# Performance work log

Hardware: AMD Instinct MI355X
Metric: run time of the kernel (lower is better)

The kernel has to match this reference:

```python
import jax, jax.numpy as jnp
import numpy as np

B, T, H = 32, 2000, 512      # batch, encoder frames, d_model
L = 256                      # max label length (padded output tokens)
THRESHOLD = 0.95


def setup_inputs() -> dict:
    key = jax.random.key(0)
    k1, k2, k3 = jax.random.split(key, 3)
    hidden = jax.random.normal(k1, (B, T, H), dtype=jnp.float32)
    alphas = jax.random.uniform(k2, (B, T), dtype=jnp.float32)
    target_lengths = jax.random.randint(k3, (B,), 64, L + 1)
    return {"hidden": hidden, "alphas": alphas, "target_lengths": target_lengths}


def _cif(hidden, alphas):
    # Continuous integrate-and-fire scan over time.
    Bt, Tt, Ht = hidden.shape

    def step(carry, xs):
        integrate, frame = carry          # [B], [B,H]
        alpha, h = xs                     # [B], [B,H]
        dist_completion = 1.0 - integrate
        integrate = integrate + alpha
        fire = integrate >= THRESHOLD     # [B] bool
        cur = jnp.where(fire, dist_completion, alpha)
        remainds = alpha - cur
        frame_out = frame + cur[:, None] * h
        integ_next = jnp.where(fire, integrate - 1.0, integrate)
        frame_next = jnp.where(fire[:, None], remainds[:, None] * h, frame_out)
        return (integ_next, frame_next), (frame_out, fire)

    init = (jnp.zeros((Bt,), hidden.dtype), jnp.zeros((Bt, Ht), hidden.dtype))
    _, (frames, fires) = jax.lax.scan(step, init, (alphas.T, jnp.swapaxes(hidden, 0, 1)))
    frames = jnp.swapaxes(frames, 0, 1)   # [B,T,H] accumulated frame at each step
    fires = fires.T                        # [B,T] fire events

    # Gather fired frames into padded [B, L, H] token tensor (vectorized scatter).
    tok = jnp.cumsum(fires.astype(jnp.int32), axis=1) - 1   # token index per fired frame
    valid = fires & (tok >= 0) & (tok < L)
    out = jnp.zeros((Bt, L, Ht), hidden.dtype)
    b_idx = jnp.arange(Bt)[:, None]
    out = out.at[b_idx, jnp.clip(tok, 0, L - 1)].add(
        frames * valid[..., None].astype(hidden.dtype))
    return out


def reference(hidden, alphas, target_lengths):
    # Rescale alphas so each row sums to target length (noise term omitted).
    num = target_lengths.astype(alphas.dtype)
    alphas = alphas * (num / alphas.sum(-1))[:, None]
    return _cif(hidden, alphas)
```

## Files before the change

kernel.cpp:

```cpp
#include <hip/hip_runtime.h>

#define BB 32
#define TT 2000
#define TTP 2048
#define HH 512
#define LL 256
#define THRESH 0.95f


__global__ __launch_bounds__(256) void cif_scan_kernel(
    const float* __restrict__ alphas, const int* __restrict__ tlen,
    float* __restrict__ w_self, float* __restrict__ w_next,
    int* __restrict__ fire_pos, int* __restrict__ nfires)
{
    const int b = blockIdx.x;
    __shared__ float sa[TTP];
    __shared__ double red[256];

    const float* arow = alphas + b * TT;
    double s = 0.0;
    for (int t = threadIdx.x; t < TT; t += 256) {
        float a = arow[t];
        sa[t] = a;
        s += (double)a;
    }
    if (threadIdx.x < TTP - TT) sa[TT + threadIdx.x] = 0.0f;
    red[threadIdx.x] = s;
    __syncthreads();
    for (int off = 128; off > 0; off >>= 1) {
        if (threadIdx.x < off) red[threadIdx.x] += red[threadIdx.x + off];
        __syncthreads();
    }
    const float sumf = (float)red[0];
    const float scale = (float)tlen[b] / sumf;
    for (int t = threadIdx.x; t < TT; t += 256) sa[t] = sa[t] * scale;
    __syncthreads();

    if (threadIdx.x == 0) {
        const float4* sa4 = (const float4*)sa;
        float4* ws4 = (float4*)(w_self + b * TT);
        float4* wn4 = (float4*)(w_next + b * TT);
        int* fp = fire_pos + b * LL;
        float integ = 0.0f;
        int nf = 0;

        float4 buf[16];
        #pragma unroll
        for (int i = 0; i < 16; ++i) buf[i] = sa4[i];

        for (int c = 0; c < 32; ++c) {
            float4 nbuf[16];
            if (c < 31) {
                #pragma unroll
                for (int i = 0; i < 16; ++i) nbuf[i] = sa4[(c + 1) * 16 + i];
            }
            #pragma unroll
            for (int i = 0; i < 16; ++i) {
                const int g = c * 16 + i;
                if (g < TT / 4) {
                    const float av[4] = {buf[i].x, buf[i].y, buf[i].z, buf[i].w};
                    float wsv[4], wnv[4];
                    #pragma unroll
                    for (int j = 0; j < 4; ++j) {
                        const float a = av[j];
                        const float dist = 1.0f - integ;
                        float ii = integ + a;
                        const bool fire = (ii >= THRESH);
                        wsv[j] = fire ? dist : a;
                        wnv[j] = fire ? (a - wsv[j]) : 0.0f;
                        if (fire) {
                            if (nf < LL) fp[nf] = g * 4 + j;
                            nf++;
                            ii -= 1.0f;
                        }
                        integ = ii;
                    }
                    ws4[g] = make_float4(wsv[0], wsv[1], wsv[2], wsv[3]);
                    wn4[g] = make_float4(wnv[0], wnv[1], wnv[2], wnv[3]);
                }
            }
            #pragma unroll
            for (int i = 0; i < 16; ++i) buf[i] = nbuf[i];
        }
        nfires[b] = (nf < LL) ? nf : LL;
    }
}

__global__ __launch_bounds__(128) void cif_gather_kernel(
    const float* __restrict__ hidden,
    const float* __restrict__ w_self, const float* __restrict__ w_next,
    const int* __restrict__ fire_pos, const int* __restrict__ nfires,
    float* __restrict__ out)
{
    const int l = blockIdx.x;
    const int b = blockIdx.y;
    const int tid = threadIdx.x;

    float4 acc = make_float4(0.f, 0.f, 0.f, 0.f);
    const int F = nfires[b];
    if (l < F) {
        const int e = fire_pos[b * LL + l];
        const float* hb = hidden + (size_t)b * TT * HH + (size_t)tid * 4;
        const float* wsb = w_self + b * TT;
        int t0;
        if (l == 0) {
            t0 = 0;
        } else {
            const int sprev = fire_pos[b * LL + l - 1];
            const float w = w_next[b * TT + sprev];
            const float4 hv0 = *(const float4*)(hb + (size_t)sprev * HH);
            acc.x = w * hv0.x; acc.y = w * hv0.y; acc.z = w * hv0.z; acc.w = w * hv0.w;
            t0 = sprev + 1;
        }
        int t = t0;
        float w = wsb[t];
        float4 hv = *(const float4*)(hb + (size_t)t * HH);
        while (t < e) {
            const float wN = wsb[t + 1];
            const float4 hN = *(const float4*)(hb + (size_t)(t + 1) * HH);
            acc.x += w * hv.x; acc.y += w * hv.y;
            acc.z += w * hv.z; acc.w += w * hv.w;
            w = wN; hv = hN; ++t;
        }
        acc.x += w * hv.x; acc.y += w * hv.y;
        acc.z += w * hv.z; acc.w += w * hv.w;
    }
    *(float4*)(out + ((size_t)b * LL + l) * HH + (size_t)tid * 4) = acc;
}

extern "C" void kernel_launch(void* const* d_in, const int* in_sizes, int n_in,
                              void* d_out, int out_size, void* d_ws, size_t ws_size,
                              hipStream_t stream) {
    const float* hidden = (const float*)d_in[0];
    const float* alphas = (const float*)d_in[1];
    const int*   tlen   = (const int*)d_in[2];
    float* out = (float*)d_out;

    float* w_self = (float*)d_ws;
    float* w_next = w_self + BB * TT;
    int* fire_pos = (int*)(w_next + BB * TT);
    int* nfires   = fire_pos + BB * LL;

    cif_scan_kernel<<<BB, 256, 0, stream>>>(alphas, tlen, w_self, w_next,
                                            fire_pos, nfires);
    cif_gather_kernel<<<dim3(LL, BB), 128, 0, stream>>>(hidden, w_self, w_next,
                                                        fire_pos, nfires, out);
}
```

Measured before the change: 300.3 us.

## Run CIF scan as one lane per batch row and record compact fire events

The scan kernel becomes a single block that first reduces the alpha sums for all rows, then gives each of 32 lanes one batch row to scan sequentially from global memory with a prefetch buffer. Instead of writing per-frame self and next weights, it stores one compact record per fire holding the position, the completion weight and the remainder. The gather kernel recomputes the interior weights from the alphas and the scale. This cuts workspace writes and moves the serial scans into one wave running side by side, but all rows now share a single CU, and alpha loads come from global memory rather than LDS.

```diff
diff --git a/kernel.cpp b/kernel.cpp
--- a/kernel.cpp
+++ b/kernel.cpp
@@ -2,7 +2,6 @@
 
 #define BB 32
 #define TT 2000
-#define TTP 2048
 #define HH 512
 #define LL 256
 #define THRESH 0.95f
@@ -10,87 +9,90 @@
 
 __global__ __launch_bounds__(256) void cif_scan_kernel(
     const float* __restrict__ alphas, const int* __restrict__ tlen,
-    float* __restrict__ w_self, float* __restrict__ w_next,
-    int* __restrict__ fire_pos, int* __restrict__ nfires)
+    float* __restrict__ scale_out, int* __restrict__ nfires,
+    int4* __restrict__ rec)
 {
-    const int b = blockIdx.x;
-    __shared__ float sa[TTP];
-    __shared__ double red[256];
+    __shared__ double red[8][256];
+    __shared__ float sscale[BB];
+    const int tid = threadIdx.x;
 
-    const float* arow = alphas + b * TT;
-    double s = 0.0;
-    for (int t = threadIdx.x; t < TT; t += 256) {
-        float a = arow[t];
-        sa[t] = a;
-        s += (double)a;
-    }
-    if (threadIdx.x < TTP - TT) sa[TT + threadIdx.x] = 0.0f;
-    red[threadIdx.x] = s;
-    __syncthreads();
-    for (int off = 128; off > 0; off >>= 1) {
-        if (threadIdx.x < off) red[threadIdx.x] += red[threadIdx.x + off];
+    for (int p = 0; p < 4; ++p) {
+        for (int bb = 0; bb < 8; ++bb) {
+            const int b = p * 8 + bb;
+            const float* arow = alphas + b * TT;
+            double s = 0.0;
+            for (int t = tid; t < TT; t += 256) s += (double)arow[t];
+            red[bb][tid] = s;
+        }
+        __syncthreads();
+        for (int off = 128; off > 0; off >>= 1) {
+            if (tid < off) {
+                #pragma unroll
+                for (int bb = 0; bb < 8; ++bb)
+                    red[bb][tid] += red[bb][tid + off];
+            }
+            __syncthreads();
+        }
+        if (tid < 8) {
+            const int b = p * 8 + tid;
+            const float sumf = (float)red[tid][0];
+            const float sc = (float)tlen[b] / sumf;
+            sscale[b] = sc;
+            scale_out[b] = sc;
+        }
         __syncthreads();
     }
-    const float sumf = (float)red[0];
-    const float scale = (float)tlen[b] / sumf;
-    for (int t = threadIdx.x; t < TT; t += 256) sa[t] = sa[t] * scale;
-    __syncthreads();
 
-    if (threadIdx.x == 0) {
-        const float4* sa4 = (const float4*)sa;
-        float4* ws4 = (float4*)(w_self + b * TT);
-        float4* wn4 = (float4*)(w_next + b * TT);
-        int* fp = fire_pos + b * LL;
-        float integ = 0.0f;
-        int nf = 0;
+    if (tid >= 32) return;
+    const int b = tid;
+    const float sc = sscale[b];
+    const float4* a4 = (const float4*)(alphas + b * TT);
+    int4* rb = rec + b * LL;
 
-        float4 buf[16];
+    float4 buf[8];
+    #pragma unroll
+    for (int i = 0; i < 8; ++i) buf[i] = a4[i];
+
+    float integ = 0.0f;
+    int nf = 0;
+    for (int cg = 0; cg < 63; ++cg) {
         #pragma unroll
-        for (int i = 0; i < 16; ++i) buf[i] = sa4[i];
-
-        for (int c = 0; c < 32; ++c) {
-            float4 nbuf[16];
-            if (c < 31) {
+        for (int i = 0; i < 8; ++i) {
+            const int g = cg * 8 + i;
+            if (g < TT / 4) {
+                float4 c = buf[i];
+                if (g + 8 < TT / 4) buf[i] = a4[g + 8];
+                const float av[4] = {c.x * sc, c.y * sc, c.z * sc, c.w * sc};
                 #pragma unroll
-                for (int i = 0; i < 16; ++i) nbuf[i] = sa4[(c + 1) * 16 + i];
-            }
-            #pragma unroll
-            for (int i = 0; i < 16; ++i) {
-                const int g = c * 16 + i;
-                if (g < TT / 4) {
-                    const float av[4] = {buf[i].x, buf[i].y, buf[i].z, buf[i].w};
-                    float wsv[4], wnv[4];
-                    #pragma unroll
-                    for (int j = 0; j < 4; ++j) {
-                        const float a = av[j];
-                        const float dist = 1.0f - integ;
-                        float ii = integ + a;
-                        const bool fire = (ii >= THRESH);
-                        wsv[j] = fire ? dist : a;
-                        wnv[j] = fire ? (a - wsv[j]) : 0.0f;
-                        if (fire) {
-                            if (nf < LL) fp[nf] = g * 4 + j;
-                            nf++;
-                            ii -= 1.0f;
+                for (int j = 0; j < 4; ++j) {
+                    const float a = av[j];
+                    const float dist = 1.0f - integ;
+                    float ii = integ + a;
+                    const bool fire = (ii >= THRESH);
+                    if (fire) {
+                        if (nf < LL) {
+                            int4 r;
+                            r.x = g * 4 + j;
+                            r.y = __float_as_int(dist);
+                            r.z = __float_as_int(a - dist);
+                            r.w = 0;
+                            rb[nf] = r;
                         }
-                        integ = ii;
+                        nf++;
+                        ii -= 1.0f;
                     }
-                    ws4[g] = make_float4(wsv[0], wsv[1], wsv[2], wsv[3]);
-                    wn4[g] = make_float4(wnv[0], wnv[1], wnv[2], wnv[3]);
+                    integ = ii;
                 }
             }
-            #pragma unroll
-            for (int i = 0; i < 16; ++i) buf[i] = nbuf[i];
         }
-        nfires[b] = (nf < LL) ? nf : LL;
     }
+    nfires[b] = (nf < LL) ? nf : LL;
 }
 
 __global__ __launch_bounds__(128) void cif_gather_kernel(
-    const float* __restrict__ hidden,
-    const float* __restrict__ w_self, const float* __restrict__ w_next,
-    const int* __restrict__ fire_pos, const int* __restrict__ nfires,
-    float* __restrict__ out)
+    const float* __restrict__ hidden, const float* __restrict__ alphas,
+    const float* __restrict__ scale, const int4* __restrict__ rec,
+    const int* __restrict__ nfires, float* __restrict__ out)
 {
     const int l = blockIdx.x;
     const int b = blockIdx.y;
@@ -99,24 +101,27 @@
     float4 acc = make_float4(0.f, 0.f, 0.f, 0.f);
     const int F = nfires[b];
     if (l < F) {
-        const int e = fire_pos[b * LL + l];
+        const int4 re = rec[b * LL + l];
+        const int e = re.x;
+        const float dist = __int_as_float(re.y);
+        const float sc = scale[b];
         const float* hb = hidden + (size_t)b * TT * HH + (size_t)tid * 4;
-        const float* wsb = w_self + b * TT;
-        int t0;
-        if (l == 0) {
-            t0 = 0;
-        } else {
-            const int sprev = fire_pos[b * LL + l - 1];
-            const float w = w_next[b * TT + sprev];
-            const float4 hv0 = *(const float4*)(hb + (size_t)sprev * HH);
-            acc.x = w * hv0.x; acc.y = w * hv0.y; acc.z = w * hv0.z; acc.w = w * hv0.w;
-            t0 = sprev + 1;
+        const float* ab = alphas + b * TT;
+        int t0 = 0;
+        if (l > 0) {
+            const int4 rp = rec[b * LL + l - 1];
+            const int sp = rp.x;
+            const float rem = __int_as_float(rp.z);
+            const float4 hv0 = *(const float4*)(hb + (size_t)sp * HH);
+            acc.x = rem * hv0.x; acc.y = rem * hv0.y;
+            acc.z = rem * hv0.z; acc.w = rem * hv0.w;
+            t0 = sp + 1;
         }
         int t = t0;
-        float w = wsb[t];
+        float w = (t < e) ? ab[t] * sc : dist;
         float4 hv = *(const float4*)(hb + (size_t)t * HH);
         while (t < e) {
-            const float wN = wsb[t + 1];
+            const float wN = (t + 1 < e) ? ab[t + 1] * sc : dist;
             const float4 hN = *(const float4*)(hb + (size_t)(t + 1) * HH);
             acc.x += w * hv.x; acc.y += w * hv.y;
             acc.z += w * hv.z; acc.w += w * hv.w;
@@ -136,13 +141,11 @@
     const int*   tlen   = (const int*)d_in[2];
     float* out = (float*)d_out;
 
-    float* w_self = (float*)d_ws;
-    float* w_next = w_self + BB * TT;
-    int* fire_pos = (int*)(w_next + BB * TT);
-    int* nfires   = fire_pos + BB * LL;
+    float* scale  = (float*)d_ws;
+    int*   nfires = (int*)(scale + BB);
+    int4*  rec    = (int4*)(nfires + BB);
 
-    cif_scan_kernel<<<BB, 256, 0, stream>>>(alphas, tlen, w_self, w_next,
-                                            fire_pos, nfires);
-    cif_gather_kernel<<<dim3(LL, BB), 128, 0, stream>>>(hidden, w_self, w_next,
-                                                        fire_pos, nfires, out);
+    cif_scan_kernel<<<1, 256, 0, stream>>>(alphas, tlen, scale, nfires, rec);
+    cif_gather_kernel<<<dim3(LL, BB), 128, 0, stream>>>(hidden, alphas, scale,
+                                                        rec, nfires, out);
 }
```

Result: slower. 433.7 us (+44.4%).
